# Kernel tuning notes

Measured on AMD Instinct MI355X. Metric: run time of the kernel, lower is better.

Reference implementation:

```python
import jax, jax.numpy as jnp
import numpy as np

B, N, ND = 32, 512, 8        # batch, graph_size, node_dim
L, H, D = 4, 8, 512          # layers, heads, embed_dim
DK = D // H                  # key_dim = val_dim = 64
F = 2048                     # feed_forward_hidden
EPS = 1e-5


def setup_inputs() -> dict:
    key = jax.random.key(0)
    ks = jax.random.split(key, 16)
    u = lambda k, shape, s: jax.random.uniform(k, shape, jnp.float32, -s, s)
    x = jax.random.normal(ks[0], (B, N, ND), dtype=jnp.float32)
    mask = jax.random.randint(ks[1], (B, N, N), 0, 2).astype(jnp.int32)  # 1 = masked
    return {
        "x": x,
        "mask": mask,
        # init_embed Linear(node_dim, embed_dim)
        "We": u(ks[2], (ND, D), 1.0 / np.sqrt(ND)),
        "be": u(ks[3], (D,), 1.0 / np.sqrt(ND)),
        # per-head projections, stacked over layers; torch init: uniform(-1/sqrt(last_dim), ...)
        "Wq": u(ks[4], (L, H, D, DK), 1.0 / np.sqrt(DK)),
        "Wk": u(ks[5], (L, H, D, DK), 1.0 / np.sqrt(DK)),
        "Wv": u(ks[6], (L, H, D, DK), 1.0 / np.sqrt(DK)),
        "Wo": u(ks[7], (L, H, DK, D), 1.0 / np.sqrt(D)),
        # BatchNorm1d affine params (torch default: weight=1, bias=0)
        "g1": jnp.ones((L, D), jnp.float32), "bt1": jnp.zeros((L, D), jnp.float32),
        "g2": jnp.ones((L, D), jnp.float32), "bt2": jnp.zeros((L, D), jnp.float32),
        # FFN
        "W1": u(ks[8], (L, D, F), 1.0 / np.sqrt(D)),
        "bf1": u(ks[9], (L, F), 1.0 / np.sqrt(D)),
        "W2": u(ks[10], (L, F, D), 1.0 / np.sqrt(F)),
        "bf2": u(ks[11], (L, D), 1.0 / np.sqrt(F)),
    }


def _batch_norm(h, g, b):
    # BatchNorm1d in training mode over flattened (B*N, D), biased variance
    hf = h.reshape(-1, h.shape[-1])
    mu = hf.mean(axis=0)
    var = hf.var(axis=0)
    return (h - mu) * jax.lax.rsqrt(var + EPS) * g + b


def reference(x, mask, We, be, Wq, Wk, Wv, Wo, g1, bt1, W1, bf1, W2, bf2, g2, bt2):
    m = mask.astype(bool)[None]                      # [1,B,N,N], True = masked
    scale = 1.0 / np.sqrt(Wq.shape[-1])
    h = x @ We + be                                  # [B,N,D]
    for l in range(Wq.shape[0]):
        # hand-rolled per-head MHA (q = h, self-attention)
        Q = jnp.einsum('bnd,hdk->hbnk', h, Wq[l])
        K = jnp.einsum('bnd,hdk->hbnk', h, Wk[l])
        V = jnp.einsum('bnd,hdv->hbnv', h, Wv[l])
        scores = jnp.einsum('hbqk,hbnk->hbqn', Q, K) * scale   # [H,B,N,N]
        scores = jnp.where(m, -jnp.inf, scores)
        attn = jax.nn.softmax(scores, axis=-1)
        attn = jnp.where(m, 0.0, attn)               # second mask-zeroing pass
        heads = jnp.einsum('hbqn,hbnv->hbqv', attn, V)
        out = jnp.einsum('hbqv,hvd->bqd', heads, Wo[l])
        h = _batch_norm(h + out, g1[l], bt1[l])      # residual + BN
        ff = jax.nn.relu(h @ W1[l] + bf1[l]) @ W2[l] + bf2[l]
        h = _batch_norm(h + ff, g2[l], bt2[l])       # residual + BN
    return (h, h.mean(axis=1))
```

## Files before the change

### kernel.cpp

```cpp
#include <hip/hip_runtime.h>
#include <hip/hip_fp16.h>
#include <math.h>

#define BN_ROWS 16384
#define DIM 512
#define FF 2048
#define LAYERS 4
#define NSEQ 512
#define BATCH 32

typedef _Float16 f16;
typedef __attribute__((ext_vector_type(8))) _Float16 f16x8;
typedef __attribute__((ext_vector_type(4))) _Float16 f16x4;
typedef __attribute__((ext_vector_type(4))) float f32x4;
typedef unsigned long long u64;

__device__ __forceinline__ f32x4 mfma_f16(f16x8 a, f16x8 b, f32x4 c) {
    return __builtin_amdgcn_mfma_f32_16x16x32_f16(a, b, c, 0, 0, 0);
}
__device__ __forceinline__ void gload_lds16(const f16* g, f16* l) {
    __builtin_amdgcn_global_load_lds(
        (const __attribute__((address_space(1))) unsigned int*)g,
        (__attribute__((address_space(3))) unsigned int*)l, 16, 0, 0);
}

__global__ __launch_bounds__(256)
void pack_qkv(const float* __restrict__ Wq, const float* __restrict__ Wk,
              const float* __restrict__ Wv, f16* __restrict__ oh) {
    size_t i = (size_t)blockIdx.x * 256 + threadIdx.x;
    int d = i & 511;
    size_t rr = i >> 9;
    int row = (int)(rr % 1536);
    int lay = (int)(rr / 1536);
    int which = row >> 9, hh = (row >> 6) & 7, k = row & 63;
    const float* W = which == 0 ? Wq : which == 1 ? Wk : Wv;
    oh[i] = (f16)W[(((size_t)lay * 8 + hh) * 512 + d) * 64 + k];
}

__global__ __launch_bounds__(256)
void transpose_w(const float* __restrict__ in, f16* __restrict__ oh, int R, int C) {
    size_t i = (size_t)blockIdx.x * 256 + threadIdx.x;
    int r = (int)(i % R);
    size_t t = i / R;
    int c = (int)(t % C);
    int lay = (int)(t / C);
    oh[i] = (f16)in[((size_t)lay * R + r) * C + c];
}

__global__ __launch_bounds__(256)
void pack_mask(const int* __restrict__ mask, u64* __restrict__ pm) {
    int wid = (blockIdx.x * 256 + threadIdx.x) >> 6;
    int lane = threadIdx.x & 63;
    for (int i = 0; i < 64; i++) {
        size_t word = (size_t)wid * 64 + i;
        u64 bal = __ballot(mask[word * 64 + lane] != 0);
        if (lane == 0) pm[word] = bal;
    }
}

__global__ __launch_bounds__(512)
void embed_kernel(const float* __restrict__ x, const float* __restrict__ We,
                  const float* __restrict__ be, f16* __restrict__ h16) {
    int row = blockIdx.x, d = threadIdx.x;
    const float* xr = x + (size_t)row * 8;
    float acc = be[d];
#pragma unroll
    for (int c = 0; c < 8; c++) acc += xr[c] * We[c * DIM + d];
    h16[(size_t)row * DIM + d] = (f16)acc;
}

template<int OUT>
__global__ __launch_bounds__(256)
void gemm_f16(const f16* __restrict__ A, const f16* __restrict__ Bt,
              const float* __restrict__ bias,
              void* __restrict__ O0, void* __restrict__ O1, void* __restrict__ O2,
              int M, int N, int K) {
    __shared__ f16 As[3][4096];
    __shared__ f16 Bs[3][4096];
    const int gx = gridDim.x;
    const int nwg = gx * gridDim.y;
    const int id = blockIdx.y * gx + blockIdx.x;
    const int chunk = nwg >> 3;
    const int sid = (id & 7) * chunk + (id >> 3);
    const int row0 = (sid / gx) * 128, col0 = (sid % gx) * 128;

    const int tid = threadIdx.x, l = tid & 63, w = tid >> 6;
    const int wr = w >> 1, wc = w & 1;
    const int fr = l & 15, fq = l >> 4;
    const int srow = l >> 2;
    const int skg = ((l & 3) ^ ((l >> 3) & 3)) * 8;
    const int fqs8 = (fq ^ ((fr >> 1) & 3)) * 8;

    f32x4 acc[4][4] = {};
    const f16* Ab = A + (size_t)(row0 + w * 32 + srow) * K + skg;
    const f16* Bb = Bt + (size_t)(col0 + w * 32 + srow) * K + skg;
    const size_t a16 = (size_t)16 * K;
    const int nt = K >> 5;

    auto stage = [&](int buf, int k0) {
        gload_lds16(Ab + k0,       &As[buf][(w * 2 + 0) * 512]);
        gload_lds16(Ab + a16 + k0, &As[buf][(w * 2 + 1) * 512]);
        gload_lds16(Bb + k0,       &Bs[buf][(w * 2 + 0) * 512]);
        gload_lds16(Bb + a16 + k0, &Bs[buf][(w * 2 + 1) * 512]);
    };

    stage(0, 0);
    stage(1, 32);

    for (int kt = 0; kt < nt; kt++) {
        const int buf = kt % 3;
        if (kt + 1 < nt) asm volatile("s_waitcnt vmcnt(4)" ::: "memory");
        else             asm volatile("s_waitcnt vmcnt(0)" ::: "memory");
        __builtin_amdgcn_s_barrier();
        __builtin_amdgcn_sched_barrier(0);
        if (kt + 2 < nt) stage((kt + 2) % 3, (kt + 2) * 32);
        f16x8 a[4], b[4];
#pragma unroll
        for (int i = 0; i < 4; i++)
            a[i] = *(const f16x8*)&As[buf][(wr * 64 + i * 16 + fr) * 32 + fqs8];
#pragma unroll
        for (int j = 0; j < 4; j++)
            b[j] = *(const f16x8*)&Bs[buf][(wc * 64 + j * 16 + fr) * 32 + fqs8];
#pragma unroll
        for (int i = 0; i < 4; i++)
#pragma unroll
            for (int j = 0; j < 4; j++)
                acc[i][j] = mfma_f16(a[i], b[j], acc[i][j]);
    }

    if (OUT == 1) {
        f16* C = (f16*)O0;
#pragma unroll
        for (int j = 0; j < 4; j++) {
            int gcol = col0 + wc * 64 + j * 16 + fr;
            float bv = bias[gcol];
#pragma unroll
            for (int i = 0; i < 4; i++) {
                int gr = row0 + wr * 64 + i * 16 + fq * 4;
#pragma unroll
                for (int r = 0; r < 4; r++)
                    C[(size_t)(gr + r) * N + gcol] = (f16)fmaxf(acc[i][j][r] + bv, 0.f);
            }
        }
    } else if (OUT == 2) {
        const float SCQ = 0.18033688011112042f;
        f16* Qo = (f16*)O0; f16* Ko = (f16*)O1; f16* Vo = (f16*)O2;
#pragma unroll
        for (int j = 0; j < 4; j++) {
            int gcol = col0 + wc * 64 + j * 16 + fr;
            if (gcol < 1024) {
                bool isQ = gcol < 512;
                f16* dst = isQ ? Qo : Ko;
                float sc = isQ ? SCQ : 1.0f;
                int cc = gcol & 511;
#pragma unroll
                for (int i = 0; i < 4; i++) {
                    int gr = row0 + wr * 64 + i * 16 + fq * 4;
#pragma unroll
                    for (int r = 0; r < 4; r++)
                        dst[(size_t)(gr + r) * 512 + cc] = (f16)(acc[i][j][r] * sc);
                }
            } else {
                int hh = (gcol - 1024) >> 6, v = gcol & 63;
#pragma unroll
                for (int i = 0; i < 4; i++) {
                    int gr = row0 + wr * 64 + i * 16 + fq * 4;
                    int b = gr >> 9, n = gr & 511;
                    f16x4 sv;
#pragma unroll
                    for (int r = 0; r < 4; r++) sv[r] = (f16)acc[i][j][r];
                    *(f16x4*)&Vo[(((size_t)b * 8 + hh) * 64 + v) * 512 + n] = sv;
                }
            }
        }
    } else {
        f16* hres = (f16*)O0;
        float* st  = (float*)O1;
#pragma unroll
        for (int j = 0; j < 4; j++) {
            int gcol = col0 + wc * 64 + j * 16 + fr;
            float bv = bias ? bias[gcol] : 0.f;
            float csum = 0.f, csq = 0.f;
#pragma unroll
            for (int i = 0; i < 4; i++) {
                int gr = row0 + wr * 64 + i * 16 + fq * 4;
#pragma unroll
                for (int r = 0; r < 4; r++) {
                    size_t idx = (size_t)(gr + r) * N + gcol;
                    float v = acc[i][j][r] + bv + (float)hres[idx];
                    hres[idx] = (f16)v;
                    csum += v; csq += v * v;
                }
            }
            csum += __shfl_down(csum, 32, 64); csum += __shfl_down(csum, 16, 64);
            csq  += __shfl_down(csq,  32, 64); csq  += __shfl_down(csq,  16, 64);
            if (fq == 0) {
                atomicAdd(&st[gcol], csum);
                atomicAdd(&st[gcol + 512], csq);
            }
        }
    }
}

__global__ __launch_bounds__(256)
void attn_flash(const f16* __restrict__ Q, const f16* __restrict__ Kg,
                const f16* __restrict__ Vt, const u64* __restrict__ pmask,
                f16* __restrict__ attf) {
    int id = blockIdx.x;
    int wgid = (id & 7) * 128 + (id >> 3);
    int qc = wgid & 3;
    int gid = wgid >> 2;
    int b = gid & 31, hd = gid >> 5;

    __shared__ f16 Kl[2][4096];
    __shared__ f16 Vl[2][4096];
    __shared__ f16 Plds[4][1024];

    const int tid = threadIdx.x, w = tid >> 6, l = tid & 63;
    const int fr = l & 15, fq = l >> 4;

    const int brow = qc * 128 + w * 32;
    const size_t qbase = ((size_t)b * NSEQ + brow) * DIM + hd * 64;
    f16x8 qa[2][2];
#pragma unroll
    for (int sub = 0; sub < 2; sub++)
#pragma unroll
        for (int ks = 0; ks < 2; ks++)
            qa[sub][ks] = *(const f16x8*)(Q + qbase + (size_t)(sub * 16 + fr) * DIM + ks * 32 + fq * 8);

    const f16* ksrc = Kg + (size_t)b * NSEQ * DIM + hd * 64;
    const f16* vsrc = Vt + ((size_t)b * 8 + hd) * 64 * 512;
    const u64* mrow = pmask + ((size_t)b * NSEQ + brow) * 8;

    const int sr = tid & 63;
    const int sg0 = tid >> 6;
    const int sg1 = sg0 + 4;

    const float THR = 11.0f;

    float mu[2][4];
    f32x4 O[2][4] = {};
    f32x4 S1[2] = {};
#pragma unroll
    for (int s = 0; s < 2; s++)
#pragma unroll
        for (int r = 0; r < 4; r++) mu[s][r] = -1e30f;

    f16x8 vones;
#pragma unroll
    for (int i = 0; i < 8; i++) vones[i] = (f16)1.0f;

    char* Pb = (char*)&Plds[w][0];

    gload_lds16(ksrc + (size_t)sr * DIM + sg0 * 8, &Kl[0][tid * 8]);
    gload_lds16(ksrc + (size_t)sr * DIM + sg1 * 8, &Kl[0][2048 + tid * 8]);
    gload_lds16(vsrc + (size_t)sr * 512 + sg0 * 8, &Vl[0][tid * 8]);
    gload_lds16(vsrc + (size_t)sr * 512 + sg1 * 8, &Vl[0][2048 + tid * 8]);

    for (int c = 0; c < 8; c++) {
        const int buf = c & 1;
        __syncthreads();
        if (c < 7) {
            const int n1 = (c + 1) * 64;
            gload_lds16(ksrc + (size_t)(n1 + sr) * DIM + sg0 * 8, &Kl[buf ^ 1][tid * 8]);
            gload_lds16(ksrc + (size_t)(n1 + sr) * DIM + sg1 * 8, &Kl[buf ^ 1][2048 + tid * 8]);
            gload_lds16(vsrc + (size_t)sr * 512 + n1 + sg0 * 8,   &Vl[buf ^ 1][tid * 8]);
            gload_lds16(vsrc + (size_t)sr * 512 + n1 + sg1 * 8,   &Vl[buf ^ 1][2048 + tid * 8]);
        }

        f16x8 kb[4][2];
#pragma unroll
        for (int nt = 0; nt < 4; nt++)
#pragma unroll
            for (int ks = 0; ks < 2; ks++)
                kb[nt][ks] = *(const f16x8*)&Kl[buf][(ks * 4 + fq) * 512 + (nt * 16 + fr) * 8];

        f32x4 ps[2][4];
#pragma unroll
        for (int sub = 0; sub < 2; sub++)
#pragma unroll
            for (int nt = 0; nt < 4; nt++) {
                f32x4 a = {};
                a = mfma_f16(qa[sub][0], kb[nt][0], a);
                a = mfma_f16(qa[sub][1], kb[nt][1], a);
                ps[sub][nt] = a;
            }
#pragma unroll
        for (int sub = 0; sub < 2; sub++)
#pragma unroll
            for (int rr = 0; rr < 4; rr++) {
                u64 bits = mrow[(size_t)(sub * 16 + fq * 4 + rr) * 8 + c];
#pragma unroll
                for (int nt = 0; nt < 4; nt++)
                    if ((bits >> (nt * 16 + fr)) & 1ull) ps[sub][nt][rr] = -INFINITY;
            }

        f16x8 vb[4][2];
#pragma unroll
        for (int vt = 0; vt < 4; vt++)
#pragma unroll
            for (int ks = 0; ks < 2; ks++)
                vb[vt][ks] = *(const f16x8*)&Vl[buf][(ks * 4 + fq) * 512 + (vt * 16 + fr) * 8];

#pragma unroll
        for (int sub = 0; sub < 2; sub++) {
            float lmax[4];
#pragma unroll
            for (int rr = 0; rr < 4; rr++)
                lmax[rr] = fmaxf(fmaxf(ps[sub][0][rr], ps[sub][1][rr]),
                                 fmaxf(ps[sub][2][rr], ps[sub][3][rr]));
            bool over = (lmax[0] > mu[sub][0] + THR) | (lmax[1] > mu[sub][1] + THR) |
                        (lmax[2] > mu[sub][2] + THR) | (lmax[3] > mu[sub][3] + THR);
            if (__any(over)) {
#pragma unroll
                for (int rr = 0; rr < 4; rr++) {
                    float v = lmax[rr];
#pragma unroll
                    for (int msk = 1; msk < 16; msk <<= 1)
                        v = fmaxf(v, __shfl_xor(v, msk, 64));
                    float mn = fmaxf(mu[sub][rr], v);
                    float sc = exp2f(mu[sub][rr] - mn);
                    mu[sub][rr] = mn;
                    S1[sub][rr] *= sc;
#pragma unroll
                    for (int vt = 0; vt < 4; vt++)
                        O[sub][vt][rr] *= sc;
                }
            }
#pragma unroll
            for (int nt = 0; nt < 4; nt++)
#pragma unroll
                for (int rr = 0; rr < 4; rr++)
                    ps[sub][nt][rr] = exp2f(ps[sub][nt][rr] - mu[sub][rr]);
#pragma unroll
            for (int nt = 0; nt < 4; nt++)
#pragma unroll
                for (int rr = 0; rr < 4; rr++) {
                    int row = fq * 4 + rr;
                    int byte = ((row * 64 + nt * 16 + fr) * 2) ^ ((row & 7) << 4);
                    *(f16*)(Pb + byte) = (f16)ps[sub][nt][rr];
                }
            f16x8 pa[2];
#pragma unroll
            for (int ks = 0; ks < 2; ks++) {
                int byte = ((fr * 64 + ks * 32 + fq * 8) * 2) ^ ((fr & 7) << 4);
                pa[ks] = *(const f16x8*)(Pb + byte);
            }
            S1[sub] = mfma_f16(pa[0], vones, S1[sub]);
            S1[sub] = mfma_f16(pa[1], vones, S1[sub]);
#pragma unroll
            for (int vt = 0; vt < 4; vt++) {
                O[sub][vt] = mfma_f16(pa[0], vb[vt][0], O[sub][vt]);
                O[sub][vt] = mfma_f16(pa[1], vb[vt][1], O[sub][vt]);
            }
        }
    }
#pragma unroll
    for (int sub = 0; sub < 2; sub++) {
        float inv[4];
#pragma unroll
        for (int rr = 0; rr < 4; rr++) inv[rr] = 1.f / S1[sub][rr];
#pragma unroll
        for (int vt = 0; vt < 4; vt++)
#pragma unroll
            for (int rr = 0; rr < 4; rr++) {
                float v = O[sub][vt][rr] * inv[rr];
                size_t idx = ((size_t)b * NSEQ + brow + sub * 16 + fq * 4 + rr) * DIM
                             + hd * 64 + vt * 16 + fr;
                attf[idx] = (f16)v;
            }
    }
}

__global__ __launch_bounds__(256)
void bn_apply(f16* __restrict__ h16, const float* __restrict__ sums,
              const float* __restrict__ g, const float* __restrict__ bt,
              float* __restrict__ outp) {
    size_t i8 = (size_t)blockIdx.x * 256 + threadIdx.x;
    size_t idx = i8 * 8;
    int c = (int)(idx & (DIM - 1));
    f16x8 hv = *(f16x8*)&h16[idx];
    float o[8];
    const float invn = 1.f / BN_ROWS;
#pragma unroll
    for (int j = 0; j < 8; j++) {
        float mu = sums[c + j] * invn;
        float var = sums[DIM + c + j] * invn - mu * mu;
        o[j] = ((float)hv[j] - mu) * rsqrtf(var + 1e-5f) * g[c + j] + bt[c + j];
    }
    f16x8 s;
#pragma unroll
    for (int j = 0; j < 8; j++) s[j] = (f16)o[j];
    *(f16x8*)&h16[idx] = s;
    if (outp) {
        *(float4*)&outp[idx]     = (float4){o[0], o[1], o[2], o[3]};
        *(float4*)&outp[idx + 4] = (float4){o[4], o[5], o[6], o[7]};
    }
}

__global__ __launch_bounds__(512)
void mean_kernel(const float* __restrict__ src, float* __restrict__ out2) {
    int b = blockIdx.x, seg = blockIdx.y, d = threadIdx.x;
    float acc = 0.f;
    for (int n = seg * 64; n < seg * 64 + 64; n++)
        acc += src[((size_t)b * NSEQ + n) * DIM + d];
    atomicAdd(&out2[b * DIM + d], acc * (1.f / NSEQ));
}

extern "C" void kernel_launch(void* const* d_in, const int* in_sizes, int n_in,
                              void* d_out, int out_size, void* d_ws, size_t ws_size,
                              hipStream_t stream) {
    const float* x   = (const float*)d_in[0];
    const int*   mask= (const int*)d_in[1];
    const float* We  = (const float*)d_in[2];
    const float* be  = (const float*)d_in[3];
    const float* Wq  = (const float*)d_in[4];
    const float* Wk  = (const float*)d_in[5];
    const float* Wv  = (const float*)d_in[6];
    const float* Wo  = (const float*)d_in[7];
    const float* g1  = (const float*)d_in[8];
    const float* bt1 = (const float*)d_in[9];
    const float* g2  = (const float*)d_in[10];
    const float* bt2 = (const float*)d_in[11];
    const float* W1  = (const float*)d_in[12];
    const float* bf1 = (const float*)d_in[13];
    const float* W2  = (const float*)d_in[14];
    const float* bf2 = (const float*)d_in[15];
    float* out = (float*)d_out;

    const size_t MiB = 1ull << 20;
    const size_t M1 = (size_t)BN_ROWS * DIM;
    char* base = (char*)d_ws;
    f16*   h16   = (f16*)base;
    f16*   Qf    = (f16*)(base + 16 * MiB);
    f16*   Kf    = (f16*)(base + 32 * MiB);
    f16*   Vt    = (f16*)(base + 48 * MiB);
    f16*   attf  = (f16*)(base + 64 * MiB);
    f16*   ffh   = (f16*)(base + 16 * MiB);
    float* stats = (float*)(base + 80 * MiB);
    u64*   pmask = (u64*)(base + 80 * MiB + 65536);
    f16*   wqkv  = (f16*)(base + 82 * MiB);
    f16*   wo    = wqkv + (size_t)4 * 1536 * 512;
    f16*   w1t   = wo   + (size_t)4 * 512 * 512;
    f16*   w2t   = w1t  + (size_t)4 * 2048 * 512;

    pack_qkv<<<dim3(4 * 1536 * 512 / 256), dim3(256), 0, stream>>>(Wq, Wk, Wv, wqkv);
    transpose_w<<<dim3(4 * 512 * 512 / 256), dim3(256), 0, stream>>>(Wo, wo, 512, 512);
    transpose_w<<<dim3(4 * 512 * 2048 / 256), dim3(256), 0, stream>>>(W1, w1t, 512, 2048);
    transpose_w<<<dim3(4 * 2048 * 512 / 256), dim3(256), 0, stream>>>(W2, w2t, 2048, 512);
    pack_mask<<<dim3(512), dim3(256), 0, stream>>>(mask, pmask);
    hipMemsetAsync(out + M1, 0, BATCH * DIM * sizeof(float), stream);

    embed_kernel<<<dim3(BN_ROWS), dim3(512), 0, stream>>>(x, We, be, h16);

    for (int l = 0; l < LAYERS; l++) {
        gemm_f16<2><<<dim3(1536 / 128, 128), dim3(256), 0, stream>>>(
            h16, wqkv + (size_t)l * 1536 * 512, nullptr, Qf, Kf, Vt,
            BN_ROWS, 1536, 512);

        attn_flash<<<dim3(1024), dim3(256), 0, stream>>>(Qf, Kf, Vt, pmask, attf);

        hipMemsetAsync(stats, 0, 1024 * sizeof(float), stream);
        gemm_f16<3><<<dim3(512 / 128, 128), dim3(256), 0, stream>>>(
            attf, wo + (size_t)l * 512 * 512, nullptr, h16, stats, nullptr,
            BN_ROWS, 512, 512);
        bn_apply<<<dim3(M1 / 2048), dim3(256), 0, stream>>>(
            h16, stats, g1 + l * DIM, bt1 + l * DIM, nullptr);

        hipMemsetAsync(stats, 0, 1024 * sizeof(float), stream);
        gemm_f16<1><<<dim3(FF / 128, BN_ROWS / 128), dim3(256), 0, stream>>>(
            h16, w1t + (size_t)l * FF * DIM, bf1 + (size_t)l * FF,
            ffh, nullptr, nullptr, BN_ROWS, FF, DIM);
        gemm_f16<3><<<dim3(512 / 128, 128), dim3(256), 0, stream>>>(
            ffh, w2t + (size_t)l * DIM * FF, bf2 + (size_t)l * DIM,
            h16, stats, nullptr, BN_ROWS, 512, FF);

        float* outp = (l == LAYERS - 1) ? out : nullptr;
        bn_apply<<<dim3(M1 / 2048), dim3(256), 0, stream>>>(
            h16, stats, g2 + l * DIM, bt2 + l * DIM, outp);
    }

    mean_kernel<<<dim3(BATCH, 8), dim3(512), 0, stream>>>(out, out + M1);
}
```

Baseline: 1.187 ms.

## Rewrite flash attention with 32x32 transposed MFMA and register-resident P

Switches the attention kernel from 16x16x32 MFMA tiles to 32x32x16 MFMA with a transposed formulation (S^T = K·Q^T), so each lane owns one query row. The softmax max and rescale then need only a single cross-half shuffle, and P is repacked into the B operand with cvt_pkrtz and permlane32_swap instead of a round trip through LDS. This removes the per-wave P scratch buffer and most shuffle reductions. In exchange it uses larger accumulator fragments, which raises register pressure, and it depends on an exact lane-layout mapping and on permlane32_swap being available.

```diff
diff --git a/kernel.cpp b/kernel.cpp
--- a/kernel.cpp
+++ b/kernel.cpp
@@ -13,10 +13,18 @@
 typedef __attribute__((ext_vector_type(8))) _Float16 f16x8;
 typedef __attribute__((ext_vector_type(4))) _Float16 f16x4;
 typedef __attribute__((ext_vector_type(4))) float f32x4;
+typedef __attribute__((ext_vector_type(16))) float f32x16;
 typedef unsigned long long u64;
 
 __device__ __forceinline__ f32x4 mfma_f16(f16x8 a, f16x8 b, f32x4 c) {
     return __builtin_amdgcn_mfma_f32_16x16x32_f16(a, b, c, 0, 0, 0);
+}
+__device__ __forceinline__ f32x16 mfma32(f16x8 a, f16x8 b, f32x16 c) {
+    return __builtin_amdgcn_mfma_f32_32x32x16_f16(a, b, c, 0, 0, 0);
+}
+__device__ __forceinline__ unsigned pk2u(float x, float y) {
+    auto t = __builtin_amdgcn_cvt_pkrtz(x, y);
+    return *reinterpret_cast<unsigned*>(&t);
 }
 __device__ __forceinline__ void gload_lds16(const f16* g, f16* l) {
     __builtin_amdgcn_global_load_lds(
@@ -214,43 +222,32 @@
 
     __shared__ f16 Kl[2][4096];
     __shared__ f16 Vl[2][4096];
-    __shared__ f16 Plds[4][1024];
 
     const int tid = threadIdx.x, w = tid >> 6, l = tid & 63;
-    const int fr = l & 15, fq = l >> 4;
+    const int q = l & 31, hi = l >> 5;
 
     const int brow = qc * 128 + w * 32;
-    const size_t qbase = ((size_t)b * NSEQ + brow) * DIM + hd * 64;
-    f16x8 qa[2][2];
-#pragma unroll
-    for (int sub = 0; sub < 2; sub++)
-#pragma unroll
-        for (int ks = 0; ks < 2; ks++)
-            qa[sub][ks] = *(const f16x8*)(Q + qbase + (size_t)(sub * 16 + fr) * DIM + ks * 32 + fq * 8);
+    const size_t qrow = ((size_t)b * NSEQ + brow + q) * DIM + hd * 64;
+    f16x8 qb[4];
+#pragma unroll
+    for (int c16 = 0; c16 < 4; c16++)
+        qb[c16] = *(const f16x8*)(Q + qrow + c16 * 16 + hi * 8);
 
     const f16* ksrc = Kg + (size_t)b * NSEQ * DIM + hd * 64;
     const f16* vsrc = Vt + ((size_t)b * 8 + hd) * 64 * 512;
-    const u64* mrow = pmask + ((size_t)b * NSEQ + brow) * 8;
+    const u64* mrowq = pmask + ((size_t)b * NSEQ + brow + q) * 8;
 
     const int sr = tid & 63;
     const int sg0 = tid >> 6;
     const int sg1 = sg0 + 4;
 
     const float THR = 11.0f;
-
-    float mu[2][4];
-    f32x4 O[2][4] = {};
-    f32x4 S1[2] = {};
-#pragma unroll
-    for (int s = 0; s < 2; s++)
-#pragma unroll
-        for (int r = 0; r < 4; r++) mu[s][r] = -1e30f;
+    float mu = -1e30f;
+    f32x16 O0 = {}, O1 = {}, S1 = {};
 
     f16x8 vones;
 #pragma unroll
     for (int i = 0; i < 8; i++) vones[i] = (f16)1.0f;
-
-    char* Pb = (char*)&Plds[w][0];
 
     gload_lds16(ksrc + (size_t)sr * DIM + sg0 * 8, &Kl[0][tid * 8]);
     gload_lds16(ksrc + (size_t)sr * DIM + sg1 * 8, &Kl[0][2048 + tid * 8]);
@@ -268,107 +265,83 @@
             gload_lds16(vsrc + (size_t)sr * 512 + n1 + sg1 * 8,   &Vl[buf ^ 1][2048 + tid * 8]);
         }
 
-        f16x8 kb[4][2];
-#pragma unroll
-        for (int nt = 0; nt < 4; nt++)
-#pragma unroll
-            for (int ks = 0; ks < 2; ks++)
-                kb[nt][ks] = *(const f16x8*)&Kl[buf][(ks * 4 + fq) * 512 + (nt * 16 + fr) * 8];
-
-        f32x4 ps[2][4];
-#pragma unroll
-        for (int sub = 0; sub < 2; sub++)
-#pragma unroll
-            for (int nt = 0; nt < 4; nt++) {
-                f32x4 a = {};
-                a = mfma_f16(qa[sub][0], kb[nt][0], a);
-                a = mfma_f16(qa[sub][1], kb[nt][1], a);
-                ps[sub][nt] = a;
-            }
-#pragma unroll
-        for (int sub = 0; sub < 2; sub++)
-#pragma unroll
-            for (int rr = 0; rr < 4; rr++) {
-                u64 bits = mrow[(size_t)(sub * 16 + fq * 4 + rr) * 8 + c];
-#pragma unroll
-                for (int nt = 0; nt < 4; nt++)
-                    if ((bits >> (nt * 16 + fr)) & 1ull) ps[sub][nt][rr] = -INFINITY;
-            }
-
-        f16x8 vb[4][2];
-#pragma unroll
-        for (int vt = 0; vt < 4; vt++)
-#pragma unroll
-            for (int ks = 0; ks < 2; ks++)
-                vb[vt][ks] = *(const f16x8*)&Vl[buf][(ks * 4 + fq) * 512 + (vt * 16 + fr) * 8];
-
-#pragma unroll
-        for (int sub = 0; sub < 2; sub++) {
-            float lmax[4];
-#pragma unroll
-            for (int rr = 0; rr < 4; rr++)
-                lmax[rr] = fmaxf(fmaxf(ps[sub][0][rr], ps[sub][1][rr]),
-                                 fmaxf(ps[sub][2][rr], ps[sub][3][rr]));
-            bool over = (lmax[0] > mu[sub][0] + THR) | (lmax[1] > mu[sub][1] + THR) |
-                        (lmax[2] > mu[sub][2] + THR) | (lmax[3] > mu[sub][3] + THR);
-            if (__any(over)) {
-#pragma unroll
-                for (int rr = 0; rr < 4; rr++) {
-                    float v = lmax[rr];
-#pragma unroll
-                    for (int msk = 1; msk < 16; msk <<= 1)
-                        v = fmaxf(v, __shfl_xor(v, msk, 64));
-                    float mn = fmaxf(mu[sub][rr], v);
-                    float sc = exp2f(mu[sub][rr] - mn);
-                    mu[sub][rr] = mn;
-                    S1[sub][rr] *= sc;
-#pragma unroll
-                    for (int vt = 0; vt < 4; vt++)
-                        O[sub][vt][rr] *= sc;
-                }
-            }
-#pragma unroll
-            for (int nt = 0; nt < 4; nt++)
-#pragma unroll
-                for (int rr = 0; rr < 4; rr++)
-                    ps[sub][nt][rr] = exp2f(ps[sub][nt][rr] - mu[sub][rr]);
-#pragma unroll
-            for (int nt = 0; nt < 4; nt++)
-#pragma unroll
-                for (int rr = 0; rr < 4; rr++) {
-                    int row = fq * 4 + rr;
-                    int byte = ((row * 64 + nt * 16 + fr) * 2) ^ ((row & 7) << 4);
-                    *(f16*)(Pb + byte) = (f16)ps[sub][nt][rr];
-                }
-            f16x8 pa[2];
-#pragma unroll
-            for (int ks = 0; ks < 2; ks++) {
-                int byte = ((fr * 64 + ks * 32 + fq * 8) * 2) ^ ((fr & 7) << 4);
-                pa[ks] = *(const f16x8*)(Pb + byte);
-            }
-            S1[sub] = mfma_f16(pa[0], vones, S1[sub]);
-            S1[sub] = mfma_f16(pa[1], vones, S1[sub]);
-#pragma unroll
-            for (int vt = 0; vt < 4; vt++) {
-                O[sub][vt] = mfma_f16(pa[0], vb[vt][0], O[sub][vt]);
-                O[sub][vt] = mfma_f16(pa[1], vb[vt][1], O[sub][vt]);
-            }
-        }
-    }
-#pragma unroll
-    for (int sub = 0; sub < 2; sub++) {
-        float inv[4];
-#pragma unroll
-        for (int rr = 0; rr < 4; rr++) inv[rr] = 1.f / S1[sub][rr];
-#pragma unroll
-        for (int vt = 0; vt < 4; vt++)
-#pragma unroll
-            for (int rr = 0; rr < 4; rr++) {
-                float v = O[sub][vt][rr] * inv[rr];
-                size_t idx = ((size_t)b * NSEQ + brow + sub * 16 + fq * 4 + rr) * DIM
-                             + hd * 64 + vt * 16 + fr;
-                attf[idx] = (f16)v;
-            }
+        f32x16 ps0 = {}, ps1 = {};
+#pragma unroll
+        for (int c16 = 0; c16 < 4; c16++) {
+            f16x8 kb0 = *(const f16x8*)&Kl[buf][((c16 * 2 + hi) * 64 + q) * 8];
+            f16x8 kb1 = *(const f16x8*)&Kl[buf][((c16 * 2 + hi) * 64 + 32 + q) * 8];
+            ps0 = mfma32(kb0, qb[c16], ps0);
+            ps1 = mfma32(kb1, qb[c16], ps1);
+        }
+
+        u64 bits = mrowq[c];
+        unsigned blo = (unsigned)bits, bhi = (unsigned)(bits >> 32);
+        float p0[16], p1[16];
+#pragma unroll
+        for (int r = 0; r < 16; r++) {
+            int n0 = (r & 3) + 8 * (r >> 2) + 4 * hi;
+            p0[r] = ((blo >> n0) & 1u) ? -INFINITY : ps0[r];
+            p1[r] = ((bhi >> n0) & 1u) ? -INFINITY : ps1[r];
+        }
+
+        float lm = fmaxf(p0[0], p1[0]);
+#pragma unroll
+        for (int r = 1; r < 16; r++) lm = fmaxf(lm, fmaxf(p0[r], p1[r]));
+        if (__any(lm > mu + THR)) {
+            float other = __shfl_xor(lm, 32, 64);
+            float mn = fmaxf(mu, fmaxf(lm, other));
+            float sc = exp2f(mu - mn);
+            mu = mn;
+            S1 *= sc; O0 *= sc; O1 *= sc;
+        }
+
+#pragma unroll
+        for (int r = 0; r < 16; r++) {
+            p0[r] = exp2f(p0[r] - mu);
+            p1[r] = exp2f(p1[r] - mu);
+        }
+
+        f16x8 PA[2][2];
+#pragma unroll
+        for (int ntile = 0; ntile < 2; ntile++) {
+            const float* p = ntile ? p1 : p0;
+#pragma unroll
+            for (int m = 0; m < 2; m++) {
+                unsigned a0 = pk2u(p[m * 8 + 0], p[m * 8 + 1]);
+                unsigned b0 = pk2u(p[m * 8 + 4], p[m * 8 + 5]);
+                auto s0 = __builtin_amdgcn_permlane32_swap(a0, b0, false, false);
+                unsigned a1 = pk2u(p[m * 8 + 2], p[m * 8 + 3]);
+                unsigned b1 = pk2u(p[m * 8 + 6], p[m * 8 + 7]);
+                auto s1 = __builtin_amdgcn_permlane32_swap(a1, b1, false, false);
+                unsigned wbuf[4] = {(unsigned)s0[0], (unsigned)s1[0],
+                                    (unsigned)s0[1], (unsigned)s1[1]};
+                PA[ntile][m] = *reinterpret_cast<f16x8*>(wbuf);
+            }
+        }
+
+#pragma unroll
+        for (int ntile = 0; ntile < 2; ntile++)
+#pragma unroll
+            for (int m = 0; m < 2; m++) {
+                f16x8 pa = PA[ntile][m];
+                S1 = mfma32(vones, pa, S1);
+                int cg = ntile * 4 + m * 2 + hi;
+                f16x8 v0 = *(const f16x8*)&Vl[buf][(cg * 64 + q) * 8];
+                f16x8 v1 = *(const f16x8*)&Vl[buf][(cg * 64 + 32 + q) * 8];
+                O0 = mfma32(v0, pa, O0);
+                O1 = mfma32(v1, pa, O1);
+            }
+    }
+
+    float inv = 1.f / S1[0];
+    f16* orow = attf + ((size_t)b * NSEQ + brow + q) * DIM + hd * 64;
+#pragma unroll
+    for (int r = 0; r < 16; r += 2) {
+        int v = (r & 3) + 8 * (r >> 2) + 4 * hi;
+        unsigned w0 = pk2u(O0[r] * inv, O0[r + 1] * inv);
+        *(unsigned*)(orow + v) = w0;
+        unsigned w1 = pk2u(O1[r] * inv, O1[r + 1] * inv);
+        *(unsigned*)(orow + 32 + v) = w1;
     }
 }
 
```

Measured after the change: 1.152 ms. 2.9% less time.
